# Kernel optimization log

Hardware: AMD Instinct MI355X
Metric: run time of the kernel (lower is better)

Reference implementation:

```python
import jax, jax.numpy as jnp
import numpy as np

K = 2          # number of pool_types ('max','avg') -> mixture components
HID = 32       # selector hidden width (Conv2d(channels,32,1))
KH = KW = 3    # conv_pool kernel_size=3, padding=1


def setup_inputs() -> dict:
    key = jax.random.key(0)
    ks = jax.random.split(key, 6)
    B, C, H, W = 16, 128, 192, 192
    x = jax.random.normal(ks[0], (B, C, H, W), jnp.float32)
    # selector: 1x1 convs == linear layers on globally-pooled features
    w1 = jax.random.normal(ks[1], (HID, C), jnp.float32) * (1.0 / np.sqrt(C))
    b1 = jnp.zeros((HID,), jnp.float32)
    w2 = jax.random.normal(ks[2], (K, HID), jnp.float32) * (1.0 / np.sqrt(HID))
    b2 = jnp.zeros((K,), jnp.float32)
    # bank of K depthwise kernels: [K, out_channels=C, C//groups=1, kh, kw]
    weight_bank = jax.random.normal(ks[3], (K, C, 1, KH, KW), jnp.float32) * (1.0 / 3.0)
    bias = jax.random.normal(ks[4], (C,), jnp.float32) * 0.01
    return {"x": x, "w1": w1, "b1": b1, "w2": w2, "b2": b2,
            "weight_bank": weight_bank, "bias": bias}


def reference(x, w1, b1, w2, b2, weight_bank, bias):
    B, C, H, W = x.shape
    # --- selector head: AdaptiveAvgPool2d(1) -> 1x1 conv -> ReLU -> 1x1 conv -> softmax ---
    pooled = x.mean(axis=(2, 3))                              # [B, C]
    h = jax.nn.relu(pooled @ w1.T + b1)                       # [B, HID]
    attn = jax.nn.softmax(h @ w2.T + b2, axis=1)              # [B, K]
    # --- per-sample dynamic kernel combination ---
    # [B,K] x [K,C,1,kh,kw] -> [B,C,1,kh,kw]
    cw = jnp.einsum('bk,koihw->boihw', attn, weight_bank)
    # --- batched depthwise conv via groups = B*C (x viewed as [1, B*C, H, W]) ---
    lhs = x.reshape(1, B * C, H, W)
    rhs = cw.reshape(B * C, 1, KH, KW)
    out = jax.lax.conv_general_dilated(
        lhs, rhs,
        window_strides=(1, 1),
        padding=((1, 1), (1, 1)),
        feature_group_count=B * C,
        dimension_numbers=('NCHW', 'OIHW', 'NCHW'))
    out = out.reshape(B, C, H, W) + bias[None, :, None, None]
    return out
```

## Files before the change

kernel.cpp:

```cpp
#include <hip/hip_runtime.h>
#include <hip/hip_bf16.h>

#define B 16
#define C 128
#define H 192
#define W 192
#define HID 32
#define K 2
#define PLANE (H*W)
#define NPLANES (B*C)
#define RB 8

typedef float floatx4 __attribute__((ext_vector_type(4)));

__global__ __launch_bounds__(256) void pool_kernel(const float* __restrict__ x,
                                                   float* __restrict__ pooled) {
    const int plane = blockIdx.x;
    const float4* px4 = (const float4*)(x + (size_t)plane * PLANE);
    float s = 0.f;
    for (int i = threadIdx.x; i < PLANE / 4; i += 256) {
        float4 v = px4[i];
        s += v.x + v.y + v.z + v.w;
    }
    for (int off = 32; off; off >>= 1) s += __shfl_down(s, off, 64);
    __shared__ float wsum[4];
    const int lane = threadIdx.x & 63, wid = threadIdx.x >> 6;
    if (lane == 0) wsum[wid] = s;
    __syncthreads();
    if (threadIdx.x == 0) {
        pooled[plane] = (wsum[0] + wsum[1] + wsum[2] + wsum[3]) * (1.0f / (float)PLANE);
    }
}

__global__ __launch_bounds__(512) void selector_kernel(const float* __restrict__ pooled,
                                                       const float* __restrict__ w1,
                                                       const float* __restrict__ b1,
                                                       const float* __restrict__ w2,
                                                       const float* __restrict__ b2,
                                                       const float* __restrict__ wb,
                                                       float* __restrict__ cw) {
    __shared__ float h[B][HID];
    __shared__ float attn[B][K];
    const int tid = threadIdx.x;

    {
        const int b = tid >> 5, j = tid & 31;
        float s = b1[j];
        const float* pb = pooled + b * C;
        const float* wj = w1 + j * C;
        #pragma unroll 8
        for (int c = 0; c < C; ++c) s += pb[c] * wj[c];
        h[b][j] = fmaxf(s, 0.f);
    }
    __syncthreads();
    if (tid < B * K) {
        const int b = tid >> 1, k = tid & 1;
        float s = b2[k];
        const float* wk = w2 + k * HID;
        #pragma unroll
        for (int j = 0; j < HID; ++j) s += h[b][j] * wk[j];
        attn[b][k] = s;
    }
    __syncthreads();
    if (tid < B) {
        const float a0 = attn[tid][0], a1 = attn[tid][1];
        const float m = fmaxf(a0, a1);
        const float e0 = __expf(a0 - m), e1 = __expf(a1 - m);
        const float inv = 1.f / (e0 + e1);
        attn[tid][0] = e0 * inv;
        attn[tid][1] = e1 * inv;
    }
    __syncthreads();
    for (int i = tid; i < B * C * 9; i += 512) {
        const int b = i / (C * 9);
        const int ci = i % (C * 9);
        cw[i] = attn[b][0] * wb[ci] + attn[b][1] * wb[C * 9 + ci];
    }
}

__global__ __launch_bounds__(576) void conv_kernel(const float* __restrict__ x,
                                                   const float* __restrict__ cw,
                                                   const float* __restrict__ bias,
                                                   float* __restrict__ out) {
    const int plane = (NPLANES - 1) - (blockIdx.x >> 1);
    const int half  = blockIdx.x & 1;
    const int tid   = threadIdx.x;
    const int xq    = tid % 48;
    const int band  = tid / 48 + half * 12;
    const int c     = plane & (C - 1);

    const float* w = cw + plane * 9;
    const float w00 = w[0], w01 = w[1], w02 = w[2];
    const float w10 = w[3], w11 = w[4], w12 = w[5];
    const float w20 = w[6], w21 = w[7], w22 = w[8];
    const float bv = bias[c];

    const int x0 = xq * 4;
    const int y0 = band * RB;
    const float* px = x + (size_t)plane * PLANE;

    float acc[RB][4];
    #pragma unroll
    for (int j = 0; j < RB; ++j) {
        acc[j][0] = bv; acc[j][1] = bv; acc[j][2] = bv; acc[j][3] = bv;
    }

    #pragma unroll
    for (int i = 0; i < RB + 2; ++i) {
        const int r = y0 - 1 + i;
        float v0, v1, v2, v3, v4, v5;
        if (r >= 0 && r < H) {
            const float* rp = px + r * W + x0;
            const float4 cur = *(const float4*)rp;
            v1 = cur.x; v2 = cur.y; v3 = cur.z; v4 = cur.w;
            v0 = (x0 > 0)     ? rp[-1] : 0.f;
            v5 = (x0 + 4 < W) ? rp[4]  : 0.f;
        } else {
            v0 = v1 = v2 = v3 = v4 = v5 = 0.f;
        }
        if (i < RB) {
            acc[i][0] = fmaf(w00, v0, fmaf(w01, v1, fmaf(w02, v2, acc[i][0])));
            acc[i][1] = fmaf(w00, v1, fmaf(w01, v2, fmaf(w02, v3, acc[i][1])));
            acc[i][2] = fmaf(w00, v2, fmaf(w01, v3, fmaf(w02, v4, acc[i][2])));
            acc[i][3] = fmaf(w00, v3, fmaf(w01, v4, fmaf(w02, v5, acc[i][3])));
        }
        if (i >= 1 && i <= RB) {
            acc[i-1][0] = fmaf(w10, v0, fmaf(w11, v1, fmaf(w12, v2, acc[i-1][0])));
            acc[i-1][1] = fmaf(w10, v1, fmaf(w11, v2, fmaf(w12, v3, acc[i-1][1])));
            acc[i-1][2] = fmaf(w10, v2, fmaf(w11, v3, fmaf(w12, v4, acc[i-1][2])));
            acc[i-1][3] = fmaf(w10, v3, fmaf(w11, v4, fmaf(w12, v5, acc[i-1][3])));
        }
        if (i >= 2) {
            acc[i-2][0] = fmaf(w20, v0, fmaf(w21, v1, fmaf(w22, v2, acc[i-2][0])));
            acc[i-2][1] = fmaf(w20, v1, fmaf(w21, v2, fmaf(w22, v3, acc[i-2][1])));
            acc[i-2][2] = fmaf(w20, v2, fmaf(w21, v3, fmaf(w22, v4, acc[i-2][2])));
            acc[i-2][3] = fmaf(w20, v3, fmaf(w21, v4, fmaf(w22, v5, acc[i-2][3])));
        }
    }

    float* po = out + (size_t)plane * PLANE + y0 * W + x0;
    #pragma unroll
    for (int j = 0; j < RB; ++j) {
        floatx4 o = { acc[j][0], acc[j][1], acc[j][2], acc[j][3] };
        __builtin_nontemporal_store(o, (floatx4*)(po + j * W));
    }
}

extern "C" void kernel_launch(void* const* d_in, const int* in_sizes, int n_in,
                              void* d_out, int out_size, void* d_ws, size_t ws_size,
                              hipStream_t stream) {
    const float* x    = (const float*)d_in[0];
    const float* w1   = (const float*)d_in[1];
    const float* b1   = (const float*)d_in[2];
    const float* w2   = (const float*)d_in[3];
    const float* b2   = (const float*)d_in[4];
    const float* wb   = (const float*)d_in[5];
    const float* bias = (const float*)d_in[6];
    float* out = (float*)d_out;

    float* pooled = (float*)d_ws;
    float* cw     = pooled + NPLANES;

    pool_kernel<<<NPLANES, 256, 0, stream>>>(x, pooled);
    selector_kernel<<<1, 512, 0, stream>>>(pooled, w1, b1, w2, b2, wb, cw);
    conv_kernel<<<NPLANES * 2, 576, 0, stream>>>(x, cw, bias, out);
}
```

Measured before the change: 203.2 us.

## Pipeline pooling and conv across plane chunks with per-block selector recompute

Replaces the three kernels (pool, selector, conv) with a single fused kernel launched five times over chunks of 512 planes. Each launch after the first pools the next chunk while convolving the current one, so the reduction and conv work overlap. Each conv block recomputes its sample's selector MLP and mixed 3x3 weights, which drops the separate single-block selector launch. In exchange, every conv block repeats the small MLP, and the pooling reads the next chunk while the conv reads the current one, which may reduce L2 reuse between the two passes over x.

```diff
diff --git a/kernel.cpp b/kernel.cpp
--- a/kernel.cpp
+++ b/kernel.cpp
@@ -10,91 +10,105 @@
 #define PLANE (H*W)
 #define NPLANES (B*C)
 #define RB 8
+#define CHUNK_PLANES 512
+#define NCHUNKS 4
 
 typedef float floatx4 __attribute__((ext_vector_type(4)));
 
-__global__ __launch_bounds__(256) void pool_kernel(const float* __restrict__ x,
-                                                   float* __restrict__ pooled) {
-    const int plane = blockIdx.x;
-    const float4* px4 = (const float4*)(x + (size_t)plane * PLANE);
-    float s = 0.f;
-    for (int i = threadIdx.x; i < PLANE / 4; i += 256) {
-        float4 v = px4[i];
-        s += v.x + v.y + v.z + v.w;
-    }
-    for (int off = 32; off; off >>= 1) s += __shfl_down(s, off, 64);
-    __shared__ float wsum[4];
-    const int lane = threadIdx.x & 63, wid = threadIdx.x >> 6;
-    if (lane == 0) wsum[wid] = s;
-    __syncthreads();
-    if (threadIdx.x == 0) {
-        pooled[plane] = (wsum[0] + wsum[1] + wsum[2] + wsum[3]) * (1.0f / (float)PLANE);
-    }
-}
-
-__global__ __launch_bounds__(512) void selector_kernel(const float* __restrict__ pooled,
-                                                       const float* __restrict__ w1,
-                                                       const float* __restrict__ b1,
-                                                       const float* __restrict__ w2,
-                                                       const float* __restrict__ b2,
-                                                       const float* __restrict__ wb,
-                                                       float* __restrict__ cw) {
-    __shared__ float h[B][HID];
-    __shared__ float attn[B][K];
+__global__ __launch_bounds__(384) void fused_kernel(const float* __restrict__ x,
+                                                    const float* __restrict__ w1,
+                                                    const float* __restrict__ b1,
+                                                    const float* __restrict__ w2,
+                                                    const float* __restrict__ b2,
+                                                    const float* __restrict__ wb,
+                                                    const float* __restrict__ bias,
+                                                    float* __restrict__ pooled,
+                                                    float* __restrict__ out,
+                                                    int convBase, int poolBase,
+                                                    int doConv, int doPool) {
     const int tid = threadIdx.x;
 
-    {
-        const int b = tid >> 5, j = tid & 31;
-        float s = b1[j];
-        const float* pb = pooled + b * C;
-        const float* wj = w1 + j * C;
+    __shared__ float red[6];
+    __shared__ float sh[HID];
+    __shared__ float sAtt[K];
+    __shared__ float sw[9];
+
+    bool isPool;
+    int poolPlane = 0, convIdx = 0;
+    if (doPool && doConv) {
+        isPool = ((blockIdx.x & 3) == 3);
+        poolPlane = poolBase + (blockIdx.x >> 2);
+        convIdx = (blockIdx.x >> 2) * 3 + (blockIdx.x & 3);
+    } else if (doPool) {
+        isPool = true;
+        poolPlane = poolBase + blockIdx.x;
+    } else {
+        isPool = false;
+        convIdx = blockIdx.x;
+    }
+
+    if (isPool) {
+        const float4* px4 = (const float4*)(x + (size_t)poolPlane * PLANE);
+        float s = 0.f;
+        #pragma unroll
+        for (int it = 0; it < PLANE / 4 / 384; ++it) {
+            float4 v = px4[tid + it * 384];
+            s += v.x + v.y + v.z + v.w;
+        }
+        for (int off = 32; off; off >>= 1) s += __shfl_down(s, off, 64);
+        const int lane = tid & 63, wid = tid >> 6;
+        if (lane == 0) red[wid] = s;
+        __syncthreads();
+        if (tid == 0) {
+            float t = red[0] + red[1] + red[2] + red[3] + red[4] + red[5];
+            pooled[poolPlane] = t * (1.0f / (float)PLANE);
+        }
+        return;
+    }
+
+    const int plane = convBase + convIdx / 3;
+    const int seg   = convIdx % 3;
+    const int c     = plane & (C - 1);
+    const int smp   = plane >> 7;
+
+    if (tid < HID) {
+        float s = b1[tid];
+        const float* pb = pooled + smp * C;
+        const float* wj = w1 + tid * C;
         #pragma unroll 8
-        for (int c = 0; c < C; ++c) s += pb[c] * wj[c];
-        h[b][j] = fmaxf(s, 0.f);
+        for (int cc = 0; cc < C; ++cc) s += pb[cc] * wj[cc];
+        sh[tid] = fmaxf(s, 0.f);
     }
     __syncthreads();
-    if (tid < B * K) {
-        const int b = tid >> 1, k = tid & 1;
-        float s = b2[k];
-        const float* wk = w2 + k * HID;
+    if (tid < K) {
+        float s = b2[tid];
+        const float* wk = w2 + tid * HID;
         #pragma unroll
-        for (int j = 0; j < HID; ++j) s += h[b][j] * wk[j];
-        attn[b][k] = s;
+        for (int j = 0; j < HID; ++j) s += sh[j] * wk[j];
+        sAtt[tid] = s;
     }
     __syncthreads();
-    if (tid < B) {
-        const float a0 = attn[tid][0], a1 = attn[tid][1];
+    if (tid == 0) {
+        const float a0 = sAtt[0], a1 = sAtt[1];
         const float m = fmaxf(a0, a1);
         const float e0 = __expf(a0 - m), e1 = __expf(a1 - m);
         const float inv = 1.f / (e0 + e1);
-        attn[tid][0] = e0 * inv;
-        attn[tid][1] = e1 * inv;
+        sAtt[0] = e0 * inv;
+        sAtt[1] = e1 * inv;
     }
     __syncthreads();
-    for (int i = tid; i < B * C * 9; i += 512) {
-        const int b = i / (C * 9);
-        const int ci = i % (C * 9);
-        cw[i] = attn[b][0] * wb[ci] + attn[b][1] * wb[C * 9 + ci];
+    if (tid < 9) {
+        sw[tid] = sAtt[0] * wb[c * 9 + tid] + sAtt[1] * wb[C * 9 + c * 9 + tid];
     }
-}
+    __syncthreads();
 
-__global__ __launch_bounds__(576) void conv_kernel(const float* __restrict__ x,
-                                                   const float* __restrict__ cw,
-                                                   const float* __restrict__ bias,
-                                                   float* __restrict__ out) {
-    const int plane = (NPLANES - 1) - (blockIdx.x >> 1);
-    const int half  = blockIdx.x & 1;
-    const int tid   = threadIdx.x;
-    const int xq    = tid % 48;
-    const int band  = tid / 48 + half * 12;
-    const int c     = plane & (C - 1);
-
-    const float* w = cw + plane * 9;
-    const float w00 = w[0], w01 = w[1], w02 = w[2];
-    const float w10 = w[3], w11 = w[4], w12 = w[5];
-    const float w20 = w[6], w21 = w[7], w22 = w[8];
+    const float w00 = sw[0], w01 = sw[1], w02 = sw[2];
+    const float w10 = sw[3], w11 = sw[4], w12 = sw[5];
+    const float w20 = sw[6], w21 = sw[7], w22 = sw[8];
     const float bv = bias[c];
 
+    const int xq   = tid % 48;
+    const int band = tid / 48 + seg * 8;
     const int x0 = xq * 4;
     const int y0 = band * RB;
     const float* px = x + (size_t)plane * PLANE;
@@ -159,9 +173,20 @@
     float* out = (float*)d_out;
 
     float* pooled = (float*)d_ws;
-    float* cw     = pooled + NPLANES;
 
-    pool_kernel<<<NPLANES, 256, 0, stream>>>(x, pooled);
-    selector_kernel<<<1, 512, 0, stream>>>(pooled, w1, b1, w2, b2, wb, cw);
-    conv_kernel<<<NPLANES * 2, 576, 0, stream>>>(x, cw, bias, out);
+    fused_kernel<<<CHUNK_PLANES, 384, 0, stream>>>(
+        x, w1, b1, w2, b2, wb, bias, pooled, out,
+        0, 0, 0, 1);
+
+    for (int c = 0; c < NCHUNKS - 1; ++c) {
+        fused_kernel<<<CHUNK_PLANES * 4, 384, 0, stream>>>(
+            x, w1, b1, w2, b2, wb, bias, pooled, out,
+            c * CHUNK_PLANES, (c + 1) * CHUNK_PLANES,
+            1, 1);
+    }
+
+    fused_kernel<<<CHUNK_PLANES * 3, 384, 0, stream>>>(
+        x, w1, b1, w2, b2, wb, bias, pooled, out,
+        (NCHUNKS - 1) * CHUNK_PLANES, 0,
+        1, 0);
 }
```

Result: slower. 216.2 us (+6.4%).

## Stage conv input tiles in LDS with 32-row segments per block

Applied to the files above, without the earlier changes.

The depthwise conv kernel now has each 384-thread block load a 34-row halo tile of one plane into shared memory with coalesced float4 loads, then compute 4 output rows per thread from that tile. Before, threads read straight from global memory with overlapping halo rows and unaligned neighbour loads. The aim is fewer redundant global reads and better coalescing. In exchange it adds a __syncthreads, shared-memory traffic, and more blocks with less work each. The padded stride of 196 floats is meant to limit bank conflicts.

```diff
diff --git a/kernel.cpp b/kernel.cpp
--- a/kernel.cpp
+++ b/kernel.cpp
@@ -9,7 +9,12 @@
 #define K 2
 #define PLANE (H*W)
 #define NPLANES (B*C)
-#define RB 8
+
+#define TBLK 384
+#define TROWS 32
+#define SROWS 34
+#define LDST 196
+#define SEGS (H / TROWS)
 
 typedef float floatx4 __attribute__((ext_vector_type(4)));
 
@@ -78,16 +83,18 @@
     }
 }
 
-__global__ __launch_bounds__(576) void conv_kernel(const float* __restrict__ x,
-                                                   const float* __restrict__ cw,
-                                                   const float* __restrict__ bias,
-                                                   float* __restrict__ out) {
-    const int plane = (NPLANES - 1) - (blockIdx.x >> 1);
-    const int half  = blockIdx.x & 1;
+__global__ __launch_bounds__(TBLK) void conv_kernel(const float* __restrict__ x,
+                                                    const float* __restrict__ cw,
+                                                    const float* __restrict__ bias,
+                                                    float* __restrict__ out) {
+    __shared__ float lds[SROWS * LDST];
+
+    const int bid   = blockIdx.x;
+    const int plane = bid / SEGS;
+    const int seg   = bid % SEGS;
     const int tid   = threadIdx.x;
-    const int xq    = tid % 48;
-    const int band  = tid / 48 + half * 12;
     const int c     = plane & (C - 1);
+    const int y0    = seg * TROWS;
 
     const float* w = cw + plane * 9;
     const float w00 = w[0], w01 = w[1], w02 = w[2];
@@ -95,36 +102,48 @@
     const float w20 = w[6], w21 = w[7], w22 = w[8];
     const float bv = bias[c];
 
-    const int x0 = xq * 4;
-    const int y0 = band * RB;
-    const float* px = x + (size_t)plane * PLANE;
+    const float4* px4 = (const float4*)(x + (size_t)plane * PLANE);
+    float4* lds4 = (float4*)lds;
+    #pragma unroll
+    for (int k = 0; k < 5; ++k) {
+        const int idx = tid + k * TBLK;
+        if (idx < SROWS * 48) {
+            const int row  = idx / 48;
+            const int col4 = idx % 48;
+            const int gRow = y0 - 1 + row;
+            float4 v = make_float4(0.f, 0.f, 0.f, 0.f);
+            if (gRow >= 0 && gRow < H) v = px4[gRow * 48 + col4];
+            lds4[row * 49 + col4] = v;
+        }
+    }
+    __syncthreads();
 
-    float acc[RB][4];
+    const int xq   = tid % 48;
+    const int band = tid / 48;
+    const int x0   = xq * 4;
+
+    float acc[4][4];
     #pragma unroll
-    for (int j = 0; j < RB; ++j) {
+    for (int j = 0; j < 4; ++j) {
         acc[j][0] = bv; acc[j][1] = bv; acc[j][2] = bv; acc[j][3] = bv;
     }
 
     #pragma unroll
-    for (int i = 0; i < RB + 2; ++i) {
-        const int r = y0 - 1 + i;
-        float v0, v1, v2, v3, v4, v5;
-        if (r >= 0 && r < H) {
-            const float* rp = px + r * W + x0;
-            const float4 cur = *(const float4*)rp;
-            v1 = cur.x; v2 = cur.y; v3 = cur.z; v4 = cur.w;
-            v0 = (x0 > 0)     ? rp[-1] : 0.f;
-            v5 = (x0 + 4 < W) ? rp[4]  : 0.f;
-        } else {
-            v0 = v1 = v2 = v3 = v4 = v5 = 0.f;
-        }
-        if (i < RB) {
+    for (int i = 0; i < 6; ++i) {
+        const int sr = band * 4 + i;
+        const float* lr = lds + sr * LDST;
+        const floatx4 cur = *(const floatx4*)(lr + x0);
+        const float v0 = (xq > 0)  ? lr[x0 - 1] : 0.f;
+        const float v5 = (xq < 47) ? lr[x0 + 4] : 0.f;
+        const float v1 = cur.x, v2 = cur.y, v3 = cur.z, v4 = cur.w;
+
+        if (i < 4) {
             acc[i][0] = fmaf(w00, v0, fmaf(w01, v1, fmaf(w02, v2, acc[i][0])));
             acc[i][1] = fmaf(w00, v1, fmaf(w01, v2, fmaf(w02, v3, acc[i][1])));
             acc[i][2] = fmaf(w00, v2, fmaf(w01, v3, fmaf(w02, v4, acc[i][2])));
             acc[i][3] = fmaf(w00, v3, fmaf(w01, v4, fmaf(w02, v5, acc[i][3])));
         }
-        if (i >= 1 && i <= RB) {
+        if (i >= 1 && i <= 4) {
             acc[i-1][0] = fmaf(w10, v0, fmaf(w11, v1, fmaf(w12, v2, acc[i-1][0])));
             acc[i-1][1] = fmaf(w10, v1, fmaf(w11, v2, fmaf(w12, v3, acc[i-1][1])));
             acc[i-1][2] = fmaf(w10, v2, fmaf(w11, v3, fmaf(w12, v4, acc[i-1][2])));
@@ -138,9 +157,9 @@
         }
     }
 
-    float* po = out + (size_t)plane * PLANE + y0 * W + x0;
+    float* po = out + (size_t)plane * PLANE + (y0 + band * 4) * W + x0;
     #pragma unroll
-    for (int j = 0; j < RB; ++j) {
+    for (int j = 0; j < 4; ++j) {
         floatx4 o = { acc[j][0], acc[j][1], acc[j][2], acc[j][3] };
         __builtin_nontemporal_store(o, (floatx4*)(po + j * W));
     }
@@ -163,5 +182,5 @@
 
     pool_kernel<<<NPLANES, 256, 0, stream>>>(x, pooled);
     selector_kernel<<<1, 512, 0, stream>>>(pooled, w1, b1, w2, b2, wb, cw);
-    conv_kernel<<<NPLANES * 2, 576, 0, stream>>>(x, cw, bias, out);
+    conv_kernel<<<NPLANES * SEGS, TBLK, 0, stream>>>(x, cw, bias, out);
 }
```

Result: faster. 163.0 us, median of 2 (-19.8%).
